# Kernel optimization log

Hardware: AMD Instinct MI355X
Metric: run time of the kernel (lower is better)

The kernel has to match this reference:

```python
import jax, jax.numpy as jnp
import numpy as np

VOCAB = 4194304
EMBED = 128
BATCH = 16384
NUM_DENSE = 13
NUM_CAT = 26
BOT_DIMS = (512, 256, 128)
TOP_DIMS = (1024, 1024, 512, 256, 1)


def _dense_params(key, fan_in, fan_out):
    kw, kb = jax.random.split(key)
    w = jax.random.normal(kw, (fan_in, fan_out), jnp.float32) * np.sqrt(2.0 / (fan_in + fan_out))
    b = jax.random.normal(kb, (fan_out,), jnp.float32) * np.sqrt(1.0 / fan_out)
    return w, b


def setup_inputs() -> dict:
    key = jax.random.key(0)
    ks = jax.random.split(key, 16)
    inp = {}
    inp['x_dense'] = jax.random.normal(ks[0], (BATCH, NUM_DENSE), jnp.float32)
    inp['x_cat'] = jax.random.randint(ks[1], (BATCH, NUM_CAT), 0, VOCAB, dtype=jnp.int32)
    # embedding table: uniform(0,1) * 1/sqrt(vocab)
    inp['embedding_table'] = jax.random.uniform(ks[2], (VOCAB, EMBED), jnp.float32) * np.float32(1.0 / np.sqrt(VOCAB))
    # bottom MLP params
    fan_in = NUM_DENSE
    for i, d in enumerate(BOT_DIMS):
        w, b = _dense_params(ks[3 + i], fan_in, d)
        inp[f'w_bot{i}'], inp[f'b_bot{i}'] = w, b
        fan_in = d
    # top MLP params; input dim = embed_dim + n_triu(27) = 128 + 378 = 506
    n_feat = 1 + NUM_CAT  # 27
    fan_in = EMBED + n_feat * (n_feat + 1) // 2
    for i, d in enumerate(TOP_DIMS):
        w, b = _dense_params(ks[8 + i], fan_in, d)
        inp[f'w_top{i}'], inp[f'b_top{i}'] = w, b
        fan_in = d
    return inp


def _forward(x_dense, x_cat, embedding_table,
             w_bot0, b_bot0, w_bot1, b_bot1, w_bot2, b_bot2,
             w_top0, b_top0, w_top1, b_top1, w_top2, b_top2,
             w_top3, b_top3, w_top4, b_top4):
    B = x_dense.shape[0]
    # bottom MLP
    h = x_dense
    for w, b in ((w_bot0, b_bot0), (w_bot1, b_bot1), (w_bot2, b_bot2)):
        h = jax.nn.relu(h @ w + b)
    bot_out = h  # [B, 128]
    feat = bot_out.reshape(B, -1, EMBED)  # [B, 1, 128]
    # embedding gather (irregular access)
    idx = (x_cat.reshape(-1) % VOCAB)
    emb = embedding_table[idx].reshape(B, NUM_CAT, EMBED)  # [B, 26, 128]
    stack = jnp.concatenate([feat, emb], axis=1)  # [B, 27, 128]
    # self interaction + upper-triangular (incl. diagonal) extraction
    xact = jnp.einsum('bnd,bmd->bnm', stack, stack)  # [B, 27, 27]
    i, j = jnp.triu_indices(stack.shape[1])
    inter = xact[:, i, j]  # [B, 378]
    top = jnp.concatenate([bot_out, inter], axis=-1)  # [B, 506]
    tops = ((w_top0, b_top0), (w_top1, b_top1), (w_top2, b_top2), (w_top3, b_top3), (w_top4, b_top4))
    for li, (w, b) in enumerate(tops):
        top = top @ w + b
        if li < len(tops) - 1:
            top = jax.nn.relu(top)
    return top  # [B, 1] logits


def reference(x_dense, x_cat, embedding_table,
              w_bot0, b_bot0, w_bot1, b_bot1, w_bot2, b_bot2,
              w_top0, b_top0, w_top1, b_top1, w_top2, b_top2,
              w_top3, b_top3, w_top4, b_top4):
    return _forward(x_dense, x_cat, embedding_table,
                    w_bot0, b_bot0, w_bot1, b_bot1, w_bot2, b_bot2,
                    w_top0, b_top0, w_top1, b_top1, w_top2, b_top2,
                    w_top3, b_top3, w_top4, b_top4)
```

## Files before the change

### kernel.cpp

```cpp
#include <hip/hip_runtime.h>
#include <cstdint>
#include <cstddef>

#define BATCH 16384
#define VOCAB_MASK (4194304 - 1)

typedef __attribute__((ext_vector_type(4))) float f32x4;
typedef __attribute__((ext_vector_type(8))) __bf16 bf16x8;
typedef __attribute__((ext_vector_type(4))) __bf16 bf16x4;

static_assert(sizeof(bf16x8) == 16, "bf16x8 must be 16 bytes");

static __device__ __forceinline__ __bf16 f2bf(float f) {
  union { float f; unsigned u; } in; in.f = f;
  unsigned r = in.u + 0x7FFF + ((in.u >> 16) & 1);
  union { unsigned short s; __bf16 b; } out; out.s = (unsigned short)(r >> 16);
  return out.b;
}
static __device__ __forceinline__ float bf2f(__bf16 b) {
  union { __bf16 b; unsigned short s; } in; in.b = b;
  union { unsigned u; float f; } out; out.u = ((unsigned)in.s) << 16;
  return out.f;
}

#define GLDS16(g, l) __builtin_amdgcn_global_load_lds( \
    (const __attribute__((address_space(1))) unsigned int*)(g), \
    (__attribute__((address_space(3))) unsigned int*)(l), 16, 0, 0)

static __device__ __forceinline__ unsigned swz16(unsigned b) {
  return b ^ ((((b >> 6) & 3u) ^ ((b >> 8) & 3u)) << 4);
}
static __device__ __forceinline__ bf16x8 lds_frag(const char* smem, unsigned base,
                                                  unsigned r, unsigned cg) {
  unsigned b = r * 64u + cg;
  return *(const bf16x8*)(smem + base + swz16(b));
}

struct TJob { const float* W; __bf16* WT; int K, N, Kp, tx, off; };
struct TJobs { TJob j[7]; };

__global__ __launch_bounds__(256) void transpose_all(TJobs js, int njobs)
{
  __shared__ float tile[64][65];
  int b = blockIdx.x;
  int ji = 0;
  #pragma unroll
  for (int i = 1; i < 7; ++i) if (i < njobs && b >= js.j[i].off) ji = i;
  const TJob jb = js.j[ji];
  int lb = b - jb.off;
  int bx = lb % jb.tx, by = lb / jb.tx;
  const int kb = bx * 64, nb = by * 64;
  const int tx = threadIdx.x & 63, ty = threadIdx.x >> 6;
  #pragma unroll
  for (int i = 0; i < 64; i += 4) {
    int k = kb + ty + i, n = nb + tx;
    tile[ty + i][tx] = (k < jb.K && n < jb.N) ? jb.W[(size_t)k * jb.N + n] : 0.f;
  }
  __syncthreads();
  #pragma unroll
  for (int i = 0; i < 64; i += 4) {
    int n = nb + ty + i, k = kb + tx;
    if (n < jb.N && k < jb.Kp) jb.WT[(size_t)n * jb.Kp + k] = f2bf(tile[tx][ty + i]);
  }
}

__global__ __launch_bounds__(256) void bottom_fused(
    const float* __restrict__ x,
    const __bf16* __restrict__ w0t, const float* __restrict__ b0,
    const __bf16* __restrict__ w1t, const float* __restrict__ b1,
    const __bf16* __restrict__ w2t, const float* __restrict__ b2,
    __bf16* __restrict__ h2out)
{
  __shared__ __bf16 h0s[32][520];
  __shared__ __bf16 h1s[32][264];
  __shared__ __bf16 As[32][40];
  const int tid = threadIdx.x, lane = tid & 63, w = tid >> 6;
  const int r0 = blockIdx.x * 32;
  const unsigned rA = lane & 15, cgw = (lane >> 4) * 8;

  for (int idx = tid; idx < 32 * 40; idx += 256) {
    int row = idx / 40, k = idx - row * 40;
    float v = (k < 13) ? x[(size_t)(r0 + row) * 13 + k] : 0.f;
    As[row][k] = f2bf(v);
  }
  __syncthreads();

  bf16x8 a00 = *(const bf16x8*)&As[rA][cgw];
  bf16x8 a01 = *(const bf16x8*)&As[rA + 16][cgw];
  #pragma unroll
  for (int p = 0; p < 2; ++p) {
    bf16x8 bv[4];
    #pragma unroll
    for (int n = 0; n < 4; ++n)
      bv[n] = *(const bf16x8*)(w0t + (size_t)(p * 256 + w * 64 + n * 16 + rA) * 32 + cgw);
    f32x4 acc[2][4] = {};
    #pragma unroll
    for (int n = 0; n < 4; ++n) {
      acc[0][n] = __builtin_amdgcn_mfma_f32_16x16x32_bf16(a00, bv[n], acc[0][n], 0, 0, 0);
      acc[1][n] = __builtin_amdgcn_mfma_f32_16x16x32_bf16(a01, bv[n], acc[1][n], 0, 0, 0);
    }
    #pragma unroll
    for (int m = 0; m < 2; ++m)
      #pragma unroll
      for (int n = 0; n < 4; ++n) {
        int col = p * 256 + w * 64 + n * 16 + (int)rA;
        float bb = b0[col];
        #pragma unroll
        for (int r = 0; r < 4; ++r) {
          int row = m * 16 + (lane >> 4) * 4 + r;
          h0s[row][col] = f2bf(fmaxf(acc[m][n][r] + bb, 0.f));
        }
      }
  }
  __syncthreads();

  f32x4 acc1[2][4] = {};
  const __bf16* w1p = w1t + (size_t)(w * 64 + rA) * 512 + cgw;
  bf16x8 c0 = *(const bf16x8*)(w1p + 0 * 8192);
  bf16x8 c1 = *(const bf16x8*)(w1p + 1 * 8192);
  bf16x8 c2 = *(const bf16x8*)(w1p + 2 * 8192);
  bf16x8 c3 = *(const bf16x8*)(w1p + 3 * 8192);
  for (int k0 = 0; k0 < 512; k0 += 32) {
    bf16x8 n0v, n1v, n2v, n3v;
    const bool more = (k0 + 32 < 512);
    if (more) {
      n0v = *(const bf16x8*)(w1p + 0 * 8192 + k0 + 32);
      n1v = *(const bf16x8*)(w1p + 1 * 8192 + k0 + 32);
      n2v = *(const bf16x8*)(w1p + 2 * 8192 + k0 + 32);
      n3v = *(const bf16x8*)(w1p + 3 * 8192 + k0 + 32);
    }
    bf16x8 av0 = *(const bf16x8*)&h0s[rA][k0 + cgw];
    bf16x8 av1 = *(const bf16x8*)&h0s[rA + 16][k0 + cgw];
    acc1[0][0] = __builtin_amdgcn_mfma_f32_16x16x32_bf16(av0, c0, acc1[0][0], 0, 0, 0);
    acc1[1][0] = __builtin_amdgcn_mfma_f32_16x16x32_bf16(av1, c0, acc1[1][0], 0, 0, 0);
    acc1[0][1] = __builtin_amdgcn_mfma_f32_16x16x32_bf16(av0, c1, acc1[0][1], 0, 0, 0);
    acc1[1][1] = __builtin_amdgcn_mfma_f32_16x16x32_bf16(av1, c1, acc1[1][1], 0, 0, 0);
    acc1[0][2] = __builtin_amdgcn_mfma_f32_16x16x32_bf16(av0, c2, acc1[0][2], 0, 0, 0);
    acc1[1][2] = __builtin_amdgcn_mfma_f32_16x16x32_bf16(av1, c2, acc1[1][2], 0, 0, 0);
    acc1[0][3] = __builtin_amdgcn_mfma_f32_16x16x32_bf16(av0, c3, acc1[0][3], 0, 0, 0);
    acc1[1][3] = __builtin_amdgcn_mfma_f32_16x16x32_bf16(av1, c3, acc1[1][3], 0, 0, 0);
    if (more) { c0 = n0v; c1 = n1v; c2 = n2v; c3 = n3v; }
  }
  #pragma unroll
  for (int m = 0; m < 2; ++m)
    #pragma unroll
    for (int n = 0; n < 4; ++n) {
      int col = w * 64 + n * 16 + (int)rA;
      float bb = b1[col];
      #pragma unroll
      for (int r = 0; r < 4; ++r) {
        int row = m * 16 + (lane >> 4) * 4 + r;
        h1s[row][col] = f2bf(fmaxf(acc1[m][n][r] + bb, 0.f));
      }
    }
  __syncthreads();

  f32x4 acc2[2][2] = {};
  const __bf16* w2p = w2t + (size_t)(w * 32 + rA) * 256 + cgw;
  bf16x8 d0 = *(const bf16x8*)(w2p + 0);
  bf16x8 d1 = *(const bf16x8*)(w2p + 4096);
  for (int k0 = 0; k0 < 256; k0 += 32) {
    bf16x8 e0, e1;
    const bool more = (k0 + 32 < 256);
    if (more) {
      e0 = *(const bf16x8*)(w2p + k0 + 32);
      e1 = *(const bf16x8*)(w2p + 4096 + k0 + 32);
    }
    bf16x8 av0 = *(const bf16x8*)&h1s[rA][k0 + cgw];
    bf16x8 av1 = *(const bf16x8*)&h1s[rA + 16][k0 + cgw];
    acc2[0][0] = __builtin_amdgcn_mfma_f32_16x16x32_bf16(av0, d0, acc2[0][0], 0, 0, 0);
    acc2[1][0] = __builtin_amdgcn_mfma_f32_16x16x32_bf16(av1, d0, acc2[1][0], 0, 0, 0);
    acc2[0][1] = __builtin_amdgcn_mfma_f32_16x16x32_bf16(av0, d1, acc2[0][1], 0, 0, 0);
    acc2[1][1] = __builtin_amdgcn_mfma_f32_16x16x32_bf16(av1, d1, acc2[1][1], 0, 0, 0);
    if (more) { d0 = e0; d1 = e1; }
  }
  #pragma unroll
  for (int m = 0; m < 2; ++m)
    #pragma unroll
    for (int n = 0; n < 2; ++n) {
      int col = w * 32 + n * 16 + (int)rA;
      float bb = b2[col];
      #pragma unroll
      for (int r = 0; r < 4; ++r) {
        int row = m * 16 + (lane >> 4) * 4 + r;
        h2out[(size_t)(r0 + row) * 128 + col] = f2bf(fmaxf(acc2[m][n][r] + bb, 0.f));
      }
    }
}

__global__ __launch_bounds__(256) void interact_mfma(
    const __bf16* __restrict__ bot, const int* __restrict__ xcat,
    const float* __restrict__ emb, __bf16* __restrict__ top_in)
{
  __shared__ __bf16 st[4][32][136];
  const int tid = threadIdx.x, lane = tid & 63, w = tid >> 6;
  const int s = blockIdx.x * 4 + w;

  const int* xr = xcat + (size_t)s * 26;
  float4 buf[13];
  #pragma unroll
  for (int i = 0; i < 13; ++i) {
    int fi = 2 * i + (lane >> 5);
    int ridx = xr[fi] & VOCAB_MASK;
    buf[i] = *(const float4*)(emb + (size_t)ridx * 128 + (lane & 31) * 4);
  }

  *(unsigned*)&st[w][0][lane * 2] = *(const unsigned*)(bot + (size_t)s * 128 + lane * 2);
  #pragma unroll
  for (int r = 27; r < 32; ++r) *(unsigned*)&st[w][r][lane * 2] = 0u;
  #pragma unroll
  for (int i = 0; i < 13; ++i) {
    int row = 1 + 2 * i + (lane >> 5);
    bf16x4 bv;
    bv[0] = f2bf(buf[i].x); bv[1] = f2bf(buf[i].y);
    bv[2] = f2bf(buf[i].z); bv[3] = f2bf(buf[i].w);
    *(bf16x4*)&st[w][row][(lane & 31) * 4] = bv;
  }

  f32x4 a00 = {}, a01 = {}, a11 = {};
  #pragma unroll
  for (int k0 = 0; k0 < 4; ++k0) {
    bf16x8 fr0 = *(const bf16x8*)&st[w][(lane & 15)][k0 * 32 + (lane >> 4) * 8];
    bf16x8 fr1 = *(const bf16x8*)&st[w][16 + (lane & 15)][k0 * 32 + (lane >> 4) * 8];
    a00 = __builtin_amdgcn_mfma_f32_16x16x32_bf16(fr0, fr0, a00, 0, 0, 0);
    a01 = __builtin_amdgcn_mfma_f32_16x16x32_bf16(fr0, fr1, a01, 0, 0, 0);
    a11 = __builtin_amdgcn_mfma_f32_16x16x32_bf16(fr1, fr1, a11, 0, 0, 0);
  }

  __bf16* op = top_in + (size_t)s * 512;
  ((unsigned*)op)[lane] = *(const unsigned*)&st[w][0][lane * 2];

  __bf16* sc = &st[w][0][0];
  if (lane < 6) sc[378 + lane] = f2bf(0.f);
  const int jc = lane & 15, rb = (lane >> 4) * 4;
  #pragma unroll
  for (int r = 0; r < 4; ++r) {
    {
      int i = rb + r, j = jc;
      if (i <= j) sc[i * 27 - i * (i - 1) / 2 + (j - i)] = f2bf(a00[r]);
    }
    {
      int i = rb + r, j = 16 + jc;
      if (j <= 26) sc[i * 27 - i * (i - 1) / 2 + (j - i)] = f2bf(a01[r]);
    }
    {
      int i = 16 + rb + r, j = 16 + jc;
      if (i <= j && j <= 26) sc[i * 27 - i * (i - 1) / 2 + (j - i)] = f2bf(a11[r]);
    }
  }
  asm volatile("s_waitcnt lgkmcnt(0)" ::: "memory");
  __builtin_amdgcn_sched_barrier(0);
  const unsigned* scd = (const unsigned*)sc;
  #pragma unroll
  for (int k = 0; k < 3; ++k)
    ((unsigned*)op)[64 + k * 64 + lane] = scd[k * 64 + lane];
}

__global__ __launch_bounds__(512, 4) void gemm_8ph_bm128(
    const __bf16* __restrict__ A, const __bf16* __restrict__ WT,
    const float* __restrict__ bias, __bf16* __restrict__ C,
    int N, int sA, int K, int gm)
{
  __shared__ __align__(16) char smem[49152];
  const int tid = threadIdx.x, lane = tid & 63, w = tid >> 6;
  const int wm = w >> 2, wn = w & 3;

  int nb = gridDim.x;
  int id = blockIdx.x;
  int swz = ((nb & 7) == 0) ? ((id & 7) * (nb >> 3) + (id >> 3)) : id;
  const int m0 = (swz % gm) * 128, n0 = (swz / gm) * 256;

  unsigned LdA; const __bf16* sApA;
  {
    unsigned L = (unsigned)w * 1024u + (unsigned)lane * 16u;
    unsigned Ls = swz16(L);
    LdA = L;
    sApA = A + (size_t)(m0 + (Ls >> 6)) * sA + ((Ls & 63) >> 1);
  }
  unsigned LdB[2]; const __bf16* sBp[2];
  #pragma unroll
  for (int h = 0; h < 2; ++h) {
    unsigned L = h * 8192u + (unsigned)w * 1024u + (unsigned)lane * 16u;
    unsigned Ls = swz16(L);
    LdB[h] = L;
    sBp[h] = WT + (size_t)(n0 + (Ls >> 6)) * K + ((Ls & 63) >> 1);
  }

  #define STAGE_A1(kt, p) { GLDS16(sApA + (kt)*32, smem + (p)*24576 + LdA); }
  #define STAGE_B2(kt, p) { GLDS16(sBp[0] + (kt)*32, smem + (p)*24576 + 8192 + LdB[0]); \
                            GLDS16(sBp[1] + (kt)*32, smem + (p)*24576 + 8192 + LdB[1]); }

  const unsigned cg = (lane >> 4) * 16u;
  const unsigned rA = (lane & 15);

  f32x4 acc[4][4] = {};
  const int iters = (K >> 5) >> 1;

  STAGE_B2(0, 0); STAGE_A1(0, 0); STAGE_B2(1, 1);
  asm volatile("s_waitcnt vmcnt(2)" ::: "memory");
  __builtin_amdgcn_s_barrier();
  __builtin_amdgcn_sched_barrier(0);

  for (int i = 0; i < iters; ++i) {
    const int t = 2 * i;
    const bool more = (i + 1 < iters);

    bf16x8 a0[2], b0[4];
    #pragma unroll
    for (int m = 0; m < 2; ++m) a0[m] = lds_frag(smem, 0, wm * 64 + m * 16 + rA, cg);
    #pragma unroll
    for (int n = 0; n < 4; ++n) b0[n] = lds_frag(smem, 8192, wn * 64 + n * 16 + rA, cg);
    STAGE_A1(t + 1, 1);
    __builtin_amdgcn_s_barrier();
    asm volatile("s_waitcnt lgkmcnt(0)" ::: "memory");
    __builtin_amdgcn_sched_barrier(0);
    __builtin_amdgcn_s_setprio(1);
    #pragma unroll
    for (int m = 0; m < 2; ++m)
      #pragma unroll
      for (int n = 0; n < 4; ++n)
        acc[m][n] = __builtin_amdgcn_mfma_f32_16x16x32_bf16(a0[m], b0[n], acc[m][n], 0, 0, 0);
    __builtin_amdgcn_s_setprio(0);
    __builtin_amdgcn_s_barrier();
    __builtin_amdgcn_sched_barrier(0);

    bf16x8 a1[2];
    #pragma unroll
    for (int m = 0; m < 2; ++m) a1[m] = lds_frag(smem, 0, wm * 64 + 32 + m * 16 + rA, cg);
    if (more) STAGE_B2(t + 2, 0);
    __builtin_amdgcn_s_barrier();
    asm volatile("s_waitcnt lgkmcnt(0)" ::: "memory");
    __builtin_amdgcn_sched_barrier(0);
    __builtin_amdgcn_s_setprio(1);
    #pragma unroll
    for (int m = 0; m < 2; ++m)
      #pragma unroll
      for (int n = 0; n < 4; ++n)
        acc[2 + m][n] = __builtin_amdgcn_mfma_f32_16x16x32_bf16(a1[m], b0[n], acc[2 + m][n], 0, 0, 0);
    __builtin_amdgcn_s_setprio(0);
    if (more) { asm volatile("s_waitcnt vmcnt(2)" ::: "memory"); }
    else      { asm volatile("s_waitcnt vmcnt(0)" ::: "memory"); }
    __builtin_amdgcn_s_barrier();
    __builtin_amdgcn_sched_barrier(0);

    bf16x8 a2[2], b2[4];
    #pragma unroll
    for (int m = 0; m < 2; ++m) a2[m] = lds_frag(smem, 24576, wm * 64 + m * 16 + rA, cg);
    #pragma unroll
    for (int n = 0; n < 4; ++n) b2[n] = lds_frag(smem, 24576 + 8192, wn * 64 + n * 16 + rA, cg);
    if (more) STAGE_A1(t + 2, 0);
    __builtin_amdgcn_s_barrier();
    asm volatile("s_waitcnt lgkmcnt(0)" ::: "memory");
    __builtin_amdgcn_sched_barrier(0);
    __builtin_amdgcn_s_setprio(1);
    #pragma unroll
    for (int m = 0; m < 2; ++m)
      #pragma unroll
      for (int n = 0; n < 4; ++n)
        acc[m][n] = __builtin_amdgcn_mfma_f32_16x16x32_bf16(a2[m], b2[n], acc[m][n], 0, 0, 0);
    __builtin_amdgcn_s_setprio(0);
    __builtin_amdgcn_s_barrier();
    __builtin_amdgcn_sched_barrier(0);

    bf16x8 a3[2];
    #pragma unroll
    for (int m = 0; m < 2; ++m) a3[m] = lds_frag(smem, 24576, wm * 64 + 32 + m * 16 + rA, cg);
    if (more) STAGE_B2(t + 3, 1);
    __builtin_amdgcn_s_barrier();
    asm volatile("s_waitcnt lgkmcnt(0)" ::: "memory");
    __builtin_amdgcn_sched_barrier(0);
    __builtin_amdgcn_s_setprio(1);
    #pragma unroll
    for (int m = 0; m < 2; ++m)
      #pragma unroll
      for (int n = 0; n < 4; ++n)
        acc[2 + m][n] = __builtin_amdgcn_mfma_f32_16x16x32_bf16(a3[m], b2[n], acc[2 + m][n], 0, 0, 0);
    __builtin_amdgcn_s_setprio(0);
    if (more) { asm volatile("s_waitcnt vmcnt(2)" ::: "memory"); }
    __builtin_amdgcn_s_barrier();
    __builtin_amdgcn_sched_barrier(0);
  }

  #pragma unroll
  for (int n = 0; n < 4; ++n) {
    int col = n0 + wn * 64 + n * 16 + (lane & 15);
    float bv = bias[col];
    #pragma unroll
    for (int m = 0; m < 4; ++m) {
      #pragma unroll
      for (int r = 0; r < 4; ++r) {
        int row = m0 + wm * 64 + m * 16 + (lane >> 4) * 4 + r;
        float v = fmaxf(acc[m][n][r] + bv, 0.f);
        C[(size_t)row * N + col] = f2bf(v);
      }
    }
  }
  #undef STAGE_A1
  #undef STAGE_B2
}

__global__ __launch_bounds__(512, 2) void gemm_8ph_n128(
    const __bf16* __restrict__ A, const __bf16* __restrict__ WT,
    const float* __restrict__ bias, __bf16* __restrict__ C,
    int N, int sA, int K, int gm)
{
  __shared__ __align__(16) char smem[49152];
  const int tid = threadIdx.x, lane = tid & 63, w = tid >> 6;
  const int wm = w >> 1, wn = w & 1;

  int nb = gridDim.x;
  int id = blockIdx.x;
  int swz = ((nb & 7) == 0) ? ((id & 7) * (nb >> 3) + (id >> 3)) : id;
  const int m0 = (swz % gm) * 256, n0 = (swz / gm) * 128;

  unsigned Ld[2]; const __bf16* sAp[2]; const __bf16* sBp0;
  #pragma unroll
  for (int h = 0; h < 2; ++h) {
    unsigned L = h * 8192u + (unsigned)w * 1024u + (unsigned)lane * 16u;
    unsigned Ls = swz16(L);
    Ld[h] = L;
    int srow = Ls >> 6, scb = Ls & 63;
    sAp[h] = A + (size_t)(m0 + srow) * sA + (scb >> 1);
  }
  {
    unsigned L = (unsigned)w * 1024u + (unsigned)lane * 16u;
    unsigned Ls = swz16(L);
    int srow = Ls >> 6, scb = Ls & 63;
    sBp0 = WT + (size_t)(n0 + srow) * K + (scb >> 1);
  }

  #define STAGE_A2(kt, p) { GLDS16(sAp[0] + (kt)*32, smem + (p)*24576 + Ld[0]); \
                            GLDS16(sAp[1] + (kt)*32, smem + (p)*24576 + Ld[1]); }
  #define STAGE_B1(kt, p) { GLDS16(sBp0 + (kt)*32, smem + (p)*24576 + 16384 + Ld[0]); }

  const unsigned cg = (lane >> 4) * 16u;
  const unsigned rA = (lane & 15);

  f32x4 acc[4][4] = {};
  const int iters = (K >> 5) >> 1;

  STAGE_B1(0, 0); STAGE_A2(0, 0); STAGE_B1(1, 1);
  asm volatile("s_waitcnt vmcnt(1)" ::: "memory");
  __builtin_amdgcn_s_barrier();
  __builtin_amdgcn_sched_barrier(0);

  for (int i = 0; i < iters; ++i) {
    const int t = 2 * i;
    const bool more = (i + 1 < iters);

    bf16x8 a0[2], b0[4];
    #pragma unroll
    for (int m = 0; m < 2; ++m) a0[m] = lds_frag(smem, 0, wm * 64 + m * 16 + rA, cg);
    #pragma unroll
    for (int n = 0; n < 4; ++n) b0[n] = lds_frag(smem, 16384, wn * 64 + n * 16 + rA, cg);
    STAGE_A2(t + 1, 1);
    __builtin_amdgcn_s_barrier();
    asm volatile("s_waitcnt lgkmcnt(0)" ::: "memory");
    __builtin_amdgcn_sched_barrier(0);
    __builtin_amdgcn_s_setprio(1);
    #pragma unroll
    for (int m = 0; m < 2; ++m)
      #pragma unroll
      for (int n = 0; n < 4; ++n)
        acc[m][n] = __builtin_amdgcn_mfma_f32_16x16x32_bf16(a0[m], b0[n], acc[m][n], 0, 0, 0);
    __builtin_amdgcn_s_setprio(0);
    __builtin_amdgcn_s_barrier();
    __builtin_amdgcn_sched_barrier(0);

    bf16x8 a1[2];
    #pragma unroll
    for (int m = 0; m < 2; ++m) a1[m] = lds_frag(smem, 0, wm * 64 + 32 + m * 16 + rA, cg);
    if (more) STAGE_B1(t + 2, 0);
    __builtin_amdgcn_s_barrier();
    asm volatile("s_waitcnt lgkmcnt(0)" ::: "memory");
    __builtin_amdgcn_sched_barrier(0);
    __builtin_amdgcn_s_setprio(1);
    #pragma unroll
    for (int m = 0; m < 2; ++m)
      #pragma unroll
      for (int n = 0; n < 4; ++n)
        acc[2 + m][n] = __builtin_amdgcn_mfma_f32_16x16x32_bf16(a1[m], b0[n], acc[2 + m][n], 0, 0, 0);
    __builtin_amdgcn_s_setprio(0);
    if (more) { asm volatile("s_waitcnt vmcnt(1)" ::: "memory"); }
    else      { asm volatile("s_waitcnt vmcnt(0)" ::: "memory"); }
    __builtin_amdgcn_s_barrier();
    __builtin_amdgcn_sched_barrier(0);

    bf16x8 a2[2], b2[4];
    #pragma unroll
    for (int m = 0; m < 2; ++m) a2[m] = lds_frag(smem, 24576, wm * 64 + m * 16 + rA, cg);
    #pragma unroll
    for (int n = 0; n < 4; ++n) b2[n] = lds_frag(smem, 24576 + 16384, wn * 64 + n * 16 + rA, cg);
    if (more) STAGE_A2(t + 2, 0);
    __builtin_amdgcn_s_barrier();
    asm volatile("s_waitcnt lgkmcnt(0)" ::: "memory");
    __builtin_amdgcn_sched_barrier(0);
    __builtin_amdgcn_s_setprio(1);
    #pragma unroll
    for (int m = 0; m < 2; ++m)
      #pragma unroll
      for (int n = 0; n < 4; ++n)
        acc[m][n] = __builtin_amdgcn_mfma_f32_16x16x32_bf16(a2[m], b2[n], acc[m][n], 0, 0, 0);
    __builtin_amdgcn_s_setprio(0);
    __builtin_amdgcn_s_barrier();
    __builtin_amdgcn_sched_barrier(0);

    bf16x8 a3[2];
    #pragma unroll
    for (int m = 0; m < 2; ++m) a3[m] = lds_frag(smem, 24576, wm * 64 + 32 + m * 16 + rA, cg);
    if (more) STAGE_B1(t + 3, 1);
    __builtin_amdgcn_s_barrier();
    asm volatile("s_waitcnt lgkmcnt(0)" ::: "memory");
    __builtin_amdgcn_sched_barrier(0);
    __builtin_amdgcn_s_setprio(1);
    #pragma unroll
    for (int m = 0; m < 2; ++m)
      #pragma unroll
      for (int n = 0; n < 4; ++n)
        acc[2 + m][n] = __builtin_amdgcn_mfma_f32_16x16x32_bf16(a3[m], b2[n], acc[2 + m][n], 0, 0, 0);
    __builtin_amdgcn_s_setprio(0);
    if (more) { asm volatile("s_waitcnt vmcnt(1)" ::: "memory"); }
    __builtin_amdgcn_s_barrier();
    __builtin_amdgcn_sched_barrier(0);
  }

  #pragma unroll
  for (int n = 0; n < 4; ++n) {
    int col = n0 + wn * 64 + n * 16 + (lane & 15);
    float bv = bias[col];
    #pragma unroll
    for (int m = 0; m < 4; ++m) {
      #pragma unroll
      for (int r = 0; r < 4; ++r) {
        int row = m0 + wm * 64 + m * 16 + (lane >> 4) * 4 + r;
        float v = fmaxf(acc[m][n][r] + bv, 0.f);
        C[(size_t)row * N + col] = f2bf(v);
      }
    }
  }
  #undef STAGE_A2
  #undef STAGE_B1
}

__global__ __launch_bounds__(256) void gemm_t3_final(
    const __bf16* __restrict__ A, const __bf16* __restrict__ WT,
    const float* __restrict__ b3, const float* __restrict__ w4,
    const float* __restrict__ b4, float* __restrict__ out)
{
  __shared__ __bf16 As[64][32];
  __shared__ __bf16 Bs[256][32];
  __shared__ float red[64][4];
  const int tid = threadIdx.x, lane = tid & 63, wid = tid >> 6;
  const int m0 = blockIdx.x * 64;
  const int srow = wid * 16 + (lane >> 2);
  const int scol = (lane & 3) * 8;
  const __bf16* Ag0 = A + (size_t)(m0 + srow) * 512 + scol;

  f32x4 acc[4][4] = {};

  for (int k0 = 0; k0 < 512; k0 += 32) {
    __syncthreads();
    GLDS16(Ag0 + k0, &As[srow][scol]);
    #pragma unroll
    for (int c = 0; c < 4; ++c) {
      int br = wid * 64 + c * 16 + (lane >> 2);
      GLDS16(WT + (size_t)br * 512 + k0 + scol, &Bs[br][scol]);
    }
    __syncthreads();

    bf16x8 af[4], bfv[4];
    #pragma unroll
    for (int m = 0; m < 4; ++m)
      af[m] = *(const bf16x8*)&As[m * 16 + (lane & 15)][(lane >> 4) * 8];
    #pragma unroll
    for (int n = 0; n < 4; ++n)
      bfv[n] = *(const bf16x8*)&Bs[wid * 64 + n * 16 + (lane & 15)][(lane >> 4) * 8];
    #pragma unroll
    for (int m = 0; m < 4; ++m)
      #pragma unroll
      for (int n = 0; n < 4; ++n)
        acc[m][n] = __builtin_amdgcn_mfma_f32_16x16x32_bf16(af[m], bfv[n], acc[m][n], 0, 0, 0);
  }

  float pd[4][4];
  #pragma unroll
  for (int m = 0; m < 4; ++m)
    #pragma unroll
    for (int r = 0; r < 4; ++r) pd[m][r] = 0.f;
  #pragma unroll
  for (int n = 0; n < 4; ++n) {
    int col = wid * 64 + n * 16 + (lane & 15);
    float bb = b3[col];
    float wc = w4[col];
    #pragma unroll
    for (int m = 0; m < 4; ++m)
      #pragma unroll
      for (int r = 0; r < 4; ++r)
        pd[m][r] += fmaxf(acc[m][n][r] + bb, 0.f) * wc;
  }
  #pragma unroll
  for (int m = 0; m < 4; ++m)
    #pragma unroll
    for (int r = 0; r < 4; ++r) {
      float s = pd[m][r];
      s += __shfl_xor(s, 1); s += __shfl_xor(s, 2);
      s += __shfl_xor(s, 4); s += __shfl_xor(s, 8);
      if ((lane & 15) == 0) red[m * 16 + (lane >> 4) * 4 + r][wid] = s;
    }
  __syncthreads();
  if (tid < 64)
    out[m0 + tid] = red[tid][0] + red[tid][1] + red[tid][2] + red[tid][3] + b4[0];
}

extern "C" void kernel_launch(void* const* d_in, const int* in_sizes, int n_in,
                              void* d_out, int out_size, void* d_ws, size_t ws_size,
                              hipStream_t stream)
{
  const float* x_dense = (const float*)d_in[0];
  const int*   x_cat   = (const int*)d_in[1];
  const float* emb     = (const float*)d_in[2];
  const float* wb[3] = {(const float*)d_in[3], (const float*)d_in[5], (const float*)d_in[7]};
  const float* bb[3] = {(const float*)d_in[4], (const float*)d_in[6], (const float*)d_in[8]};
  const float* wt[5] = {(const float*)d_in[9],  (const float*)d_in[11], (const float*)d_in[13],
                        (const float*)d_in[15], (const float*)d_in[17]};
  const float* bt[5] = {(const float*)d_in[10], (const float*)d_in[12], (const float*)d_in[14],
                        (const float*)d_in[16], (const float*)d_in[18]};
  float* out = (float*)d_out;

  char* ws = (char*)d_ws;
  const size_t MB = 1ull << 20;
  __bf16* wt_b0 = (__bf16*)(ws + 0 * MB);
  __bf16* wt_b1 = (__bf16*)(ws + 1 * MB);
  __bf16* wt_b2 = (__bf16*)(ws + 2 * MB);
  __bf16* wt_t0 = (__bf16*)(ws + 3 * MB);
  __bf16* wt_t1 = (__bf16*)(ws + 4 * MB);
  __bf16* wt_t2 = (__bf16*)(ws + 6 * MB);
  __bf16* wt_t3 = (__bf16*)(ws + 7 * MB);
  __bf16* h2     = (__bf16*)(ws + 8 * MB);
  __bf16* top_in = (__bf16*)(ws + 12 * MB);
  __bf16* t2     = (__bf16*)(ws + 12 * MB);
  __bf16* t1     = (__bf16*)(ws + 28 * MB);
  __bf16* t0     = (__bf16*)(ws + 60 * MB);

  TJobs js;
  const float* Ws[7] = {wb[0], wb[1], wb[2], wt[0], wt[1], wt[2], wt[3]};
  __bf16* WTs[7] = {wt_b0, wt_b1, wt_b2, wt_t0, wt_t1, wt_t2, wt_t3};
  int Ks[7]  = {13, 512, 256, 506, 1024, 1024, 512};
  int Ns[7]  = {512, 256, 128, 1024, 1024, 512, 256};
  int Kps[7] = {32, 512, 256, 512, 1024, 1024, 512};
  int off = 0;
  for (int i = 0; i < 7; ++i) {
    int tx = (Kps[i] + 63) / 64, ty = (Ns[i] + 63) / 64;
    js.j[i] = TJob{Ws[i], WTs[i], Ks[i], Ns[i], Kps[i], tx, off};
    off += tx * ty;
  }
  transpose_all<<<dim3(off), dim3(256), 0, stream>>>(js, 7);

  bottom_fused<<<dim3(BATCH / 32), dim3(256), 0, stream>>>(
      x_dense, wt_b0, bb[0], wt_b1, bb[1], wt_b2, bb[2], h2);

  interact_mfma<<<dim3(BATCH / 4), dim3(256), 0, stream>>>(h2, x_cat, emb, top_in);

  gemm_8ph_bm128<<<dim3(512), dim3(512), 0, stream>>>(top_in, wt_t0, bt[0], t0, 1024, 512, 512, 128);
  gemm_8ph_bm128<<<dim3(512), dim3(512), 0, stream>>>(t0, wt_t1, bt[1], t1, 1024, 1024, 1024, 128);
  gemm_8ph_n128<<<dim3(256), dim3(512), 0, stream>>>(t1, wt_t2, bt[2], t2, 512, 1024, 1024, 64);

  gemm_t3_final<<<dim3(256), dim3(256), 0, stream>>>(t2, wt_t3, bt[3], wt[4], bt[4], out);
}
```

Measured before the change: 188.9 us.

## Enlarge top-MLP GEMM tiles from 128x256 to 256x256

The first two top-MLP GEMMs now use a 256x256 output tile per block instead of 128x256. Each warp computes 128 rows, LDS grows to 64KB and occupancy drops to 2 blocks per CU, and the grid halves to 256 blocks. The aim is more reuse of each loaded fragment per MFMA and less global/LDS traffic per FLOP. The cost is more accumulator registers, lower occupancy, and a grid of 256 blocks that may not fill all CUs evenly.

```diff
diff --git a/kernel.cpp b/kernel.cpp
--- a/kernel.cpp
+++ b/kernel.cpp
@@ -256,47 +256,43 @@
     ((unsigned*)op)[64 + k * 64 + lane] = scd[k * 64 + lane];
 }
 
-__global__ __launch_bounds__(512, 4) void gemm_8ph_bm128(
+__global__ __launch_bounds__(512, 2) void gemm_8ph(
     const __bf16* __restrict__ A, const __bf16* __restrict__ WT,
     const float* __restrict__ bias, __bf16* __restrict__ C,
     int N, int sA, int K, int gm)
 {
-  __shared__ __align__(16) char smem[49152];
+  __shared__ __align__(16) char smem[65536];
   const int tid = threadIdx.x, lane = tid & 63, w = tid >> 6;
   const int wm = w >> 2, wn = w & 3;
 
   int nb = gridDim.x;
   int id = blockIdx.x;
   int swz = ((nb & 7) == 0) ? ((id & 7) * (nb >> 3) + (id >> 3)) : id;
-  const int m0 = (swz % gm) * 128, n0 = (swz / gm) * 256;
-
-  unsigned LdA; const __bf16* sApA;
-  {
-    unsigned L = (unsigned)w * 1024u + (unsigned)lane * 16u;
-    unsigned Ls = swz16(L);
-    LdA = L;
-    sApA = A + (size_t)(m0 + (Ls >> 6)) * sA + ((Ls & 63) >> 1);
-  }
-  unsigned LdB[2]; const __bf16* sBp[2];
+  const int m0 = (swz % gm) * 256, n0 = (swz / gm) * 256;
+
+  unsigned Ld[2]; const __bf16* sAp[2]; const __bf16* sBp[2];
   #pragma unroll
   for (int h = 0; h < 2; ++h) {
     unsigned L = h * 8192u + (unsigned)w * 1024u + (unsigned)lane * 16u;
     unsigned Ls = swz16(L);
-    LdB[h] = L;
-    sBp[h] = WT + (size_t)(n0 + (Ls >> 6)) * K + ((Ls & 63) >> 1);
-  }
-
-  #define STAGE_A1(kt, p) { GLDS16(sApA + (kt)*32, smem + (p)*24576 + LdA); }
-  #define STAGE_B2(kt, p) { GLDS16(sBp[0] + (kt)*32, smem + (p)*24576 + 8192 + LdB[0]); \
-                            GLDS16(sBp[1] + (kt)*32, smem + (p)*24576 + 8192 + LdB[1]); }
+    Ld[h] = L;
+    int srow = Ls >> 6, scb = Ls & 63;
+    sAp[h] = A  + (size_t)(m0 + srow) * sA + (scb >> 1);
+    sBp[h] = WT + (size_t)(n0 + srow) * K  + (scb >> 1);
+  }
+
+  #define STAGE_A(kt, p) { GLDS16(sAp[0] + (kt)*32, smem + (p)*32768 + Ld[0]); \
+                           GLDS16(sAp[1] + (kt)*32, smem + (p)*32768 + Ld[1]); }
+  #define STAGE_B(kt, p) { GLDS16(sBp[0] + (kt)*32, smem + (p)*32768 + 16384 + Ld[0]); \
+                           GLDS16(sBp[1] + (kt)*32, smem + (p)*32768 + 16384 + Ld[1]); }
 
   const unsigned cg = (lane >> 4) * 16u;
   const unsigned rA = (lane & 15);
 
-  f32x4 acc[4][4] = {};
+  f32x4 acc[8][4] = {};
   const int iters = (K >> 5) >> 1;
 
-  STAGE_B2(0, 0); STAGE_A1(0, 0); STAGE_B2(1, 1);
+  STAGE_B(0, 0); STAGE_A(0, 0); STAGE_B(1, 1);
   asm volatile("s_waitcnt vmcnt(2)" ::: "memory");
   __builtin_amdgcn_s_barrier();
   __builtin_amdgcn_sched_barrier(0);
@@ -305,18 +301,18 @@
     const int t = 2 * i;
     const bool more = (i + 1 < iters);
 
-    bf16x8 a0[2], b0[4];
-    #pragma unroll
-    for (int m = 0; m < 2; ++m) a0[m] = lds_frag(smem, 0, wm * 64 + m * 16 + rA, cg);
-    #pragma unroll
-    for (int n = 0; n < 4; ++n) b0[n] = lds_frag(smem, 8192, wn * 64 + n * 16 + rA, cg);
-    STAGE_A1(t + 1, 1);
-    __builtin_amdgcn_s_barrier();
-    asm volatile("s_waitcnt lgkmcnt(0)" ::: "memory");
-    __builtin_amdgcn_sched_barrier(0);
-    __builtin_amdgcn_s_setprio(1);
-    #pragma unroll
-    for (int m = 0; m < 2; ++m)
+    bf16x8 a0[4], b0[4];
+    #pragma unroll
+    for (int m = 0; m < 4; ++m) a0[m] = lds_frag(smem, 0, wm * 128 + m * 16 + rA, cg);
+    #pragma unroll
+    for (int n = 0; n < 4; ++n) b0[n] = lds_frag(smem, 16384, wn * 64 + n * 16 + rA, cg);
+    STAGE_A(t + 1, 1);
+    __builtin_amdgcn_s_barrier();
+    asm volatile("s_waitcnt lgkmcnt(0)" ::: "memory");
+    __builtin_amdgcn_sched_barrier(0);
+    __builtin_amdgcn_s_setprio(1);
+    #pragma unroll
+    for (int m = 0; m < 4; ++m)
       #pragma unroll
       for (int n = 0; n < 4; ++n)
         acc[m][n] = __builtin_amdgcn_mfma_f32_16x16x32_bf16(a0[m], b0[n], acc[m][n], 0, 0, 0);
@@ -324,37 +320,37 @@
     __builtin_amdgcn_s_barrier();
     __builtin_amdgcn_sched_barrier(0);
 
-    bf16x8 a1[2];
-    #pragma unroll
-    for (int m = 0; m < 2; ++m) a1[m] = lds_frag(smem, 0, wm * 64 + 32 + m * 16 + rA, cg);
-    if (more) STAGE_B2(t + 2, 0);
-    __builtin_amdgcn_s_barrier();
-    asm volatile("s_waitcnt lgkmcnt(0)" ::: "memory");
-    __builtin_amdgcn_sched_barrier(0);
-    __builtin_amdgcn_s_setprio(1);
-    #pragma unroll
-    for (int m = 0; m < 2; ++m)
-      #pragma unroll
-      for (int n = 0; n < 4; ++n)
-        acc[2 + m][n] = __builtin_amdgcn_mfma_f32_16x16x32_bf16(a1[m], b0[n], acc[2 + m][n], 0, 0, 0);
+    bf16x8 a1[4];
+    #pragma unroll
+    for (int m = 0; m < 4; ++m) a1[m] = lds_frag(smem, 0, wm * 128 + 64 + m * 16 + rA, cg);
+    if (more) STAGE_B(t + 2, 0);
+    __builtin_amdgcn_s_barrier();
+    asm volatile("s_waitcnt lgkmcnt(0)" ::: "memory");
+    __builtin_amdgcn_sched_barrier(0);
+    __builtin_amdgcn_s_setprio(1);
+    #pragma unroll
+    for (int m = 0; m < 4; ++m)
+      #pragma unroll
+      for (int n = 0; n < 4; ++n)
+        acc[4 + m][n] = __builtin_amdgcn_mfma_f32_16x16x32_bf16(a1[m], b0[n], acc[4 + m][n], 0, 0, 0);
     __builtin_amdgcn_s_setprio(0);
     if (more) { asm volatile("s_waitcnt vmcnt(2)" ::: "memory"); }
     else      { asm volatile("s_waitcnt vmcnt(0)" ::: "memory"); }
     __builtin_amdgcn_s_barrier();
     __builtin_amdgcn_sched_barrier(0);
 
-    bf16x8 a2[2], b2[4];
-    #pragma unroll
-    for (int m = 0; m < 2; ++m) a2[m] = lds_frag(smem, 24576, wm * 64 + m * 16 + rA, cg);
-    #pragma unroll
-    for (int n = 0; n < 4; ++n) b2[n] = lds_frag(smem, 24576 + 8192, wn * 64 + n * 16 + rA, cg);
-    if (more) STAGE_A1(t + 2, 0);
-    __builtin_amdgcn_s_barrier();
-    asm volatile("s_waitcnt lgkmcnt(0)" ::: "memory");
-    __builtin_amdgcn_sched_barrier(0);
-    __builtin_amdgcn_s_setprio(1);
-    #pragma unroll
-    for (int m = 0; m < 2; ++m)
+    bf16x8 a2[4], b2[4];
+    #pragma unroll
+    for (int m = 0; m < 4; ++m) a2[m] = lds_frag(smem, 32768, wm * 128 + m * 16 + rA, cg);
+    #pragma unroll
+    for (int n = 0; n < 4; ++n) b2[n] = lds_frag(smem, 32768 + 16384, wn * 64 + n * 16 + rA, cg);
+    if (more) STAGE_A(t + 2, 0);
+    __builtin_amdgcn_s_barrier();
+    asm volatile("s_waitcnt lgkmcnt(0)" ::: "memory");
+    __builtin_amdgcn_sched_barrier(0);
+    __builtin_amdgcn_s_setprio(1);
+    #pragma unroll
+    for (int m = 0; m < 4; ++m)
       #pragma unroll
       for (int n = 0; n < 4; ++n)
         acc[m][n] = __builtin_amdgcn_mfma_f32_16x16x32_bf16(a2[m], b2[n], acc[m][n], 0, 0, 0);
@@ -362,19 +358,19 @@
     __builtin_amdgcn_s_barrier();
     __builtin_amdgcn_sched_barrier(0);
 
-    bf16x8 a3[2];
-    #pragma unroll
-    for (int m = 0; m < 2; ++m) a3[m] = lds_frag(smem, 24576, wm * 64 + 32 + m * 16 + rA, cg);
-    if (more) STAGE_B2(t + 3, 1);
-    __builtin_amdgcn_s_barrier();
-    asm volatile("s_waitcnt lgkmcnt(0)" ::: "memory");
-    __builtin_amdgcn_sched_barrier(0);
-    __builtin_amdgcn_s_setprio(1);
-    #pragma unroll
-    for (int m = 0; m < 2; ++m)
-      #pragma unroll
-      for (int n = 0; n < 4; ++n)
-        acc[2 + m][n] = __builtin_amdgcn_mfma_f32_16x16x32_bf16(a3[m], b2[n], acc[2 + m][n], 0, 0, 0);
+    bf16x8 a3[4];
+    #pragma unroll
+    for (int m = 0; m < 4; ++m) a3[m] = lds_frag(smem, 32768, wm * 128 + 64 + m * 16 + rA, cg);
+    if (more) STAGE_B(t + 3, 1);
+    __builtin_amdgcn_s_barrier();
+    asm volatile("s_waitcnt lgkmcnt(0)" ::: "memory");
+    __builtin_amdgcn_sched_barrier(0);
+    __builtin_amdgcn_s_setprio(1);
+    #pragma unroll
+    for (int m = 0; m < 4; ++m)
+      #pragma unroll
+      for (int n = 0; n < 4; ++n)
+        acc[4 + m][n] = __builtin_amdgcn_mfma_f32_16x16x32_bf16(a3[m], b2[n], acc[4 + m][n], 0, 0, 0);
     __builtin_amdgcn_s_setprio(0);
     if (more) { asm volatile("s_waitcnt vmcnt(2)" ::: "memory"); }
     __builtin_amdgcn_s_barrier();
@@ -386,17 +382,17 @@
     int col = n0 + wn * 64 + n * 16 + (lane & 15);
     float bv = bias[col];
     #pragma unroll
-    for (int m = 0; m < 4; ++m) {
+    for (int m = 0; m < 8; ++m) {
       #pragma unroll
       for (int r = 0; r < 4; ++r) {
-        int row = m0 + wm * 64 + m * 16 + (lane >> 4) * 4 + r;
+        int row = m0 + wm * 128 + m * 16 + (lane >> 4) * 4 + r;
         float v = fmaxf(acc[m][n][r] + bv, 0.f);
         C[(size_t)row * N + col] = f2bf(v);
       }
     }
   }
-  #undef STAGE_A1
-  #undef STAGE_B2
+  #undef STAGE_A
+  #undef STAGE_B
 }
 
 __global__ __launch_bounds__(512, 2) void gemm_8ph_n128(
@@ -661,8 +657,8 @@
 
   interact_mfma<<<dim3(BATCH / 4), dim3(256), 0, stream>>>(h2, x_cat, emb, top_in);
 
-  gemm_8ph_bm128<<<dim3(512), dim3(512), 0, stream>>>(top_in, wt_t0, bt[0], t0, 1024, 512, 512, 128);
-  gemm_8ph_bm128<<<dim3(512), dim3(512), 0, stream>>>(t0, wt_t1, bt[1], t1, 1024, 1024, 1024, 128);
+  gemm_8ph<<<dim3(256), dim3(512), 0, stream>>>(top_in, wt_t0, bt[0], t0, 1024, 512, 512, 64);
+  gemm_8ph<<<dim3(256), dim3(512), 0, stream>>>(t0, wt_t1, bt[1], t1, 1024, 1024, 1024, 64);
   gemm_8ph_n128<<<dim3(256), dim3(512), 0, stream>>>(t1, wt_t2, bt[2], t2, 512, 1024, 1024, 64);
 
   gemm_t3_final<<<dim3(256), dim3(256), 0, stream>>>(t2, wt_t3, bt[3], wt[4], bt[4], out);
```

Result: slower. 200.6 us (+6.1%).
